# Kernel optimization log

Measured on AMD Instinct MI355X. Metric: run time of the kernel, lower is better.

Reference implementation:

```python
import jax, jax.numpy as jnp
import numpy as np

B, N, FIN, FOUT, OPD = 2048, 64, 96, 128, 48
EPS = 1e-5      # nn.LayerNorm default eps
SLOPE = 0.01    # F.leaky_relu default negative_slope (used in GAT forward)


def setup_inputs() -> dict:
    key = jax.random.key(0)
    ks = jax.random.split(key, 12)
    stdv = 1.0 / np.sqrt(FOUT)
    h = jax.random.normal(ks[0], (B, N, FIN), jnp.float32)
    # binary DAG-style adjacency (float mask, as used multiplicatively in torch)
    adj = (jax.random.uniform(ks[1], (B, N, N)) < 0.3).astype(jnp.float32)
    op_emb = jax.random.normal(ks[2], (B, N, OPD), jnp.float32)
    # DenseGraphFlow params (uniform(-stdv, stdv) per reset_parameters)
    W = jax.random.uniform(ks[3], (FIN, FOUT), jnp.float32, -stdv, stdv)
    b = jax.random.uniform(ks[4], (FOUT,), jnp.float32, -stdv, stdv)
    Wop_d = jax.random.normal(ks[5], (OPD, FOUT), jnp.float32) * 0.05
    bop_d = jnp.zeros((FOUT,), jnp.float32)
    # GraphAttentionLayer params
    Wk = jax.random.normal(ks[6], (FIN, FOUT), jnp.float32) * 0.05
    a_w = jax.random.normal(ks[7], (FOUT,), jnp.float32) * 0.05
    Wop_g = jax.random.normal(ks[8], (OPD, FOUT), jnp.float32) * 0.05
    bop_g = jnp.zeros((FOUT,), jnp.float32)
    gamma = jnp.ones((FOUT,), jnp.float32)
    beta = jnp.zeros((FOUT,), jnp.float32)
    return dict(h=h, adj=adj, op_emb=op_emb, W=W, b=b, Wop_d=Wop_d, bop_d=bop_d,
                Wk=Wk, a_w=a_w, Wop_g=Wop_g, bop_g=bop_g, gamma=gamma, beta=beta)


def reference(h, adj, op_emb, W, b, Wop_d, bop_d, Wk, a_w, Wop_g, bop_g, gamma, beta):
    # ---- DenseGraphFlow (residual=True, opattention=True) ----
    support = jnp.einsum('bnf,fo->bno', h, W)                       # [B,N,FOUT]
    gate_d = jax.nn.sigmoid(op_emb @ Wop_d + bop_d)                 # [B,N,FOUT]
    dense = gate_d * jnp.einsum('bij,bjo->bio', adj, support) + support + b

    # ---- GraphAttentionLayer (unique_attn_proj=False -> Wq=Wv=Wk) ----
    Whk = jnp.einsum('bnf,fo->bno', h, Wk)                          # [B,N,FOUT]
    # torch builds a_input[b,i,j,m] = Whk[b,j,m] * Whk[b,i,m], then projects with
    # a (Linear FOUT->1). Exactly equivalent factored form (no [B,N,N,F] tensor):
    scores = jnp.einsum('bim,bjm->bij', Whk * a_w, Whk)             # [B,N,N]
    alpha = jnp.where(scores >= 0, scores, SLOPE * scores) * adj    # leaky_relu then adj mask
    attn = jax.nn.softmax(alpha, axis=-1)                           # softmax over j (torch dim=-2 of [b,i,j,1])
    hp = jnp.einsum('bij,bjo->bio', attn, Whk)                      # aggregate values
    gate_g = jax.nn.sigmoid(op_emb @ Wop_g + bop_g)
    hp = gate_g * hp
    # LayerNorm over last dim
    mu = jnp.mean(hp, axis=-1, keepdims=True)
    var = jnp.var(hp, axis=-1, keepdims=True)
    hp = (hp - mu) / jnp.sqrt(var + EPS) * gamma + beta

    # ---- ensemble combine ----
    return (dense + hp) / 2
```

## Files before the change

### kernel.cpp

```cpp
#include <hip/hip_runtime.h>

#define NB 2048
#define NN 64
#define KFIN 96
#define KFOUT 128
#define KOPD 48

typedef __attribute__((ext_vector_type(8))) short bf8;
typedef __attribute__((ext_vector_type(4))) float f32x4;
typedef __attribute__((ext_vector_type(4))) unsigned short us4;
typedef __attribute__((ext_vector_type(2))) __bf16 bfx2;

__device__ __forceinline__ unsigned short f2bf(float f) {
  __bf16 h = (__bf16)f;
  return __builtin_bit_cast(unsigned short, h);
}
__device__ __forceinline__ float bf2f(unsigned short s) {
  unsigned int u = ((unsigned int)s) << 16;
  return __builtin_bit_cast(float, u);
}
__device__ __forceinline__ us4 pack4(float a, float b, float c, float d) {
  us4 q; q.x = f2bf(a); q.y = f2bf(b); q.z = f2bf(c); q.w = f2bf(d); return q;
}
__device__ __forceinline__ bf8 pk8(float4 a, float4 b) {
  bf8 r;
  r[0] = (short)f2bf(a.x); r[1] = (short)f2bf(a.y); r[2] = (short)f2bf(a.z); r[3] = (short)f2bf(a.w);
  r[4] = (short)f2bf(b.x); r[5] = (short)f2bf(b.y); r[6] = (short)f2bf(b.z); r[7] = (short)f2bf(b.w);
  return r;
}
__device__ __forceinline__ unsigned int pk2(float lo, float hi) {
  bfx2 v; v[0] = (__bf16)lo; v[1] = (__bf16)hi;
  return __builtin_bit_cast(unsigned int, v);
}
__device__ __forceinline__ float unpk(unsigned int p, int hi) {
  return bf2f((unsigned short)(hi ? (p >> 16) : (p & 0xffffu)));
}

__global__ void prep_weights(const float* __restrict__ W, const float* __restrict__ Wk,
                             const float* __restrict__ Wd, const float* __restrict__ Wg,
                             unsigned short* __restrict__ ws) {
  int idx = blockIdx.x * 256 + threadIdx.x;
  if (idx >= 40960) return;
  float v;
  if (idx < 24576) {
    int r  = (idx < 12288) ? idx : idx - 12288;
    const float* M = (idx < 12288) ? W : Wk;
    int nb = r / 1536, rem = r % 1536;
    int kb = rem / 512, rem2 = rem % 512;
    int l = rem2 >> 3, e = rem2 & 7;
    int o = nb * 16 + (l & 15);
    int k = kb * 32 + (l >> 4) * 8 + e;
    v = M[k * 128 + o];
  } else {
    int r  = (idx < 32768) ? idx - 24576 : idx - 32768;
    const float* M = (idx < 32768) ? Wd : Wg;
    int nb = r / 1024, rem = r % 1024;
    int kb = rem / 512, rem2 = rem % 512;
    int l = rem2 >> 3, e = rem2 & 7;
    int o = nb * 16 + (l & 15);
    int k = kb * 32 + (l >> 4) * 8 + e;
    v = (k < 48) ? M[k * 128 + o] : 0.f;
  }
  ws[idx] = f2bf(v);
}

#define LD1 68
#define LD2 132
#define LDA 68
__global__ __launch_bounds__(256, 4) void gin_fused(
    const float* __restrict__ hg, const float* __restrict__ adjg,
    const float* __restrict__ opeg, const float* __restrict__ bvec,
    const float* __restrict__ bopd, const float* __restrict__ bopg,
    const float* __restrict__ awv, const float* __restrict__ gmv,
    const float* __restrict__ btv, const unsigned short* __restrict__ ws,
    float* __restrict__ out) {
  __shared__ __align__(16) char smem[34304];
  unsigned short* buf1 = (unsigned short*)smem;
  unsigned short* buf2 = (unsigned short*)(smem + 17408);

  const int t  = threadIdx.x;
  const int b  = blockIdx.x;
  const int w  = t >> 6;
  const int l  = t & 63;
  const int lr = l & 15;
  const int lg = l >> 4;
  const int kcol = 8 * lg;
  const int arow = w * 16 + lr;
  const int rowb = w * 16 + lg * 4;

  const float* hrow = hg   + (size_t)b * (NN * KFIN) + arow * KFIN;
  const float* orow = opeg + (size_t)b * (NN * KOPD) + arow * KOPD;
  float* outp = out + (size_t)b * (NN * KFOUT);

  const unsigned short* WT  = ws;
  const unsigned short* WkT = ws + 12288;
  const unsigned short* WdT = ws + 24576;
  const unsigned short* WgT = ws + 32768;
  f32x4 zz = {0.f, 0.f, 0.f, 0.f};

  bf8 oa[2], ha[3];
  {
    float4 p0 = *(const float4*)(orow + kcol);
    float4 p1 = *(const float4*)(orow + kcol + 4);
    oa[0] = pk8(p0, p1);
    if (lg < 2) {
      float4 q0 = *(const float4*)(orow + 32 + kcol);
      float4 q1 = *(const float4*)(orow + 32 + kcol + 4);
      oa[1] = pk8(q0, q1);
    } else {
      bf8 z = {0, 0, 0, 0, 0, 0, 0, 0};
      oa[1] = z;
    }
  }
  #pragma unroll
  for (int kb = 0; kb < 3; ++kb) {
    float4 p0 = *(const float4*)(hrow + kb * 32 + kcol);
    float4 p1 = *(const float4*)(hrow + kb * 32 + kcol + 4);
    ha[kb] = pk8(p0, p1);
  }

  unsigned int gdp[8][2];
  {
    f32x4 gd[8] = {zz, zz, zz, zz, zz, zz, zz, zz};
    #pragma unroll
    for (int kb = 0; kb < 2; ++kb) {
      #pragma unroll
      for (int nb = 0; nb < 8; ++nb) {
        bf8 bb = *(const bf8*)(WdT + (nb * 2 + kb) * 512 + l * 8);
        gd[nb] = __builtin_amdgcn_mfma_f32_16x16x32_bf16(oa[kb], bb, gd[nb], 0, 0, 0);
      }
    }
    #pragma unroll
    for (int nb = 0; nb < 8; ++nb) {
      float bo = bopd[nb * 16 + lr];
      float g0 = 1.f / (1.f + __expf(-(gd[nb][0] + bo)));
      float g1 = 1.f / (1.f + __expf(-(gd[nb][1] + bo)));
      float g2 = 1.f / (1.f + __expf(-(gd[nb][2] + bo)));
      float g3 = 1.f / (1.f + __expf(-(gd[nb][3] + bo)));
      gdp[nb][0] = pk2(g0, g1); gdp[nb][1] = pk2(g2, g3);
    }
  }

  f32x4 sacc[8] = {zz, zz, zz, zz, zz, zz, zz, zz};
  #pragma unroll
  for (int kb = 0; kb < 3; ++kb) {
    #pragma unroll
    for (int nb = 0; nb < 8; ++nb) {
      bf8 bb = *(const bf8*)(WT + (nb * 3 + kb) * 512 + l * 8);
      sacc[nb] = __builtin_amdgcn_mfma_f32_16x16x32_bf16(ha[kb], bb, sacc[nb], 0, 0, 0);
    }
  }
  #pragma unroll
  for (int nb = 0; nb < 8; ++nb)
    *(us4*)(buf1 + (nb * 16 + lr) * LD1 + w * 16 + lg * 4) =
        pack4(sacc[nb][0], sacc[nb][1], sacc[nb][2], sacc[nb][3]);
  __syncthreads();

  unsigned int dnp[8][2];
  {
    const float* ajr = adjg + (size_t)b * (NN * NN) + arow * NN;
    bf8 aa[2];
    #pragma unroll
    for (int kb = 0; kb < 2; ++kb) {
      float4 p0 = *(const float4*)(ajr + kb * 32 + kcol);
      float4 p1 = *(const float4*)(ajr + kb * 32 + kcol + 4);
      aa[kb] = pk8(p0, p1);
    }
    #pragma unroll
    for (int nb = 0; nb < 8; ++nb) {
      f32x4 dacc = zz;
      #pragma unroll
      for (int kb = 0; kb < 2; ++kb) {
        bf8 bb = *(const bf8*)(buf1 + (nb * 16 + lr) * LD1 + kb * 32 + kcol);
        dacc = __builtin_amdgcn_mfma_f32_16x16x32_bf16(aa[kb], bb, dacc, 0, 0, 0);
      }
      float bc = bvec[nb * 16 + lr];
      float d0 = unpk(gdp[nb][0], 0) * dacc[0] + sacc[nb][0] + bc;
      float d1 = unpk(gdp[nb][0], 1) * dacc[1] + sacc[nb][1] + bc;
      float d2 = unpk(gdp[nb][1], 0) * dacc[2] + sacc[nb][2] + bc;
      float d3 = unpk(gdp[nb][1], 1) * dacc[3] + sacc[nb][3] + bc;
      dnp[nb][0] = pk2(d0, d1); dnp[nb][1] = pk2(d2, d3);
    }
  }

  f32x4 wacc[8] = {zz, zz, zz, zz, zz, zz, zz, zz};
  #pragma unroll
  for (int kb = 0; kb < 3; ++kb) {
    #pragma unroll
    for (int nb = 0; nb < 8; ++nb) {
      bf8 bb = *(const bf8*)(WkT + (nb * 3 + kb) * 512 + l * 8);
      wacc[nb] = __builtin_amdgcn_mfma_f32_16x16x32_bf16(ha[kb], bb, wacc[nb], 0, 0, 0);
    }
  }
  __syncthreads();

  #pragma unroll
  for (int nb = 0; nb < 8; ++nb) {
    int o = nb * 16 + lr;
    *(us4*)(buf1 + o * LD1 + w * 16 + lg * 4) =
        pack4(wacc[nb][0], wacc[nb][1], wacc[nb][2], wacc[nb][3]);
    #pragma unroll
    for (int r = 0; r < 4; ++r)
      buf2[(w * 16 + lg * 4 + r) * LD2 + o] = f2bf(wacc[nb][r]);
  }

  unsigned int ggp[8][2];
  {
    f32x4 gg[8] = {zz, zz, zz, zz, zz, zz, zz, zz};
    #pragma unroll
    for (int kb = 0; kb < 2; ++kb) {
      #pragma unroll
      for (int nb = 0; nb < 8; ++nb) {
        bf8 bb = *(const bf8*)(WgT + (nb * 2 + kb) * 512 + l * 8);
        gg[nb] = __builtin_amdgcn_mfma_f32_16x16x32_bf16(oa[kb], bb, gg[nb], 0, 0, 0);
      }
    }
    #pragma unroll
    for (int nb = 0; nb < 8; ++nb) {
      float bo = bopg[nb * 16 + lr];
      float g0 = 1.f / (1.f + __expf(-(gg[nb][0] + bo)));
      float g1 = 1.f / (1.f + __expf(-(gg[nb][1] + bo)));
      float g2 = 1.f / (1.f + __expf(-(gg[nb][2] + bo)));
      float g3 = 1.f / (1.f + __expf(-(gg[nb][3] + bo)));
      ggp[nb][0] = pk2(g0, g1); ggp[nb][1] = pk2(g2, g3);
    }
  }
  __syncthreads();

  f32x4 sc[4] = {zz, zz, zz, zz};
  #pragma unroll
  for (int kb = 0; kb < 4; ++kb) {
    bf8 ar = *(const bf8*)(buf2 + arow * LD2 + kb * 32 + kcol);
    const float4* ap = (const float4*)(awv + kb * 32 + kcol);
    float4 a0 = ap[0], a1 = ap[1];
    bf8 a;
    a[0] = (short)f2bf(bf2f((unsigned short)ar[0]) * a0.x);
    a[1] = (short)f2bf(bf2f((unsigned short)ar[1]) * a0.y);
    a[2] = (short)f2bf(bf2f((unsigned short)ar[2]) * a0.z);
    a[3] = (short)f2bf(bf2f((unsigned short)ar[3]) * a0.w);
    a[4] = (short)f2bf(bf2f((unsigned short)ar[4]) * a1.x);
    a[5] = (short)f2bf(bf2f((unsigned short)ar[5]) * a1.y);
    a[6] = (short)f2bf(bf2f((unsigned short)ar[6]) * a1.z);
    a[7] = (short)f2bf(bf2f((unsigned short)ar[7]) * a1.w);
    #pragma unroll
    for (int jb = 0; jb < 4; ++jb) {
      bf8 bb = *(const bf8*)(buf2 + (jb * 16 + lr) * LD2 + kb * 32 + kcol);
      sc[jb] = __builtin_amdgcn_mfma_f32_16x16x32_bf16(a, bb, sc[jb], 0, 0, 0);
    }
  }

  float al[4][4];
  #pragma unroll
  for (int jb = 0; jb < 4; ++jb)
    #pragma unroll
    for (int r = 0; r < 4; ++r) {
      float am = adjg[(size_t)b * (NN * NN) + (rowb + r) * NN + jb * 16 + lr];
      float s = sc[jb][r];
      al[jb][r] = (s >= 0.f ? s : 0.01f * s) * am;
    }
  #pragma unroll
  for (int r = 0; r < 4; ++r) {
    float m = fmaxf(fmaxf(al[0][r], al[1][r]), fmaxf(al[2][r], al[3][r]));
    m = fmaxf(m, __shfl_xor(m, 1));
    m = fmaxf(m, __shfl_xor(m, 2));
    m = fmaxf(m, __shfl_xor(m, 4));
    m = fmaxf(m, __shfl_xor(m, 8));
    float s0 = 0.f;
    #pragma unroll
    for (int jb = 0; jb < 4; ++jb) { float p = __expf(al[jb][r] - m); al[jb][r] = p; s0 += p; }
    s0 += __shfl_xor(s0, 1);
    s0 += __shfl_xor(s0, 2);
    s0 += __shfl_xor(s0, 4);
    s0 += __shfl_xor(s0, 8);
    float inv = 1.f / s0;
    #pragma unroll
    for (int jb = 0; jb < 4; ++jb) al[jb][r] *= inv;
  }
  __syncthreads();

  unsigned short* attn_s = buf2;
  #pragma unroll
  for (int jb = 0; jb < 4; ++jb)
    #pragma unroll
    for (int r = 0; r < 4; ++r)
      attn_s[(rowb + r) * LDA + jb * 16 + lr] = f2bf(al[jb][r]);

  f32x4 hpacc[8] = {zz, zz, zz, zz, zz, zz, zz, zz};
  #pragma unroll
  for (int kb = 0; kb < 2; ++kb) {
    bf8 a = *(const bf8*)(attn_s + arow * LDA + kb * 32 + kcol);
    #pragma unroll
    for (int nb = 0; nb < 8; ++nb) {
      bf8 bb = *(const bf8*)(buf1 + (nb * 16 + lr) * LD1 + kb * 32 + kcol);
      hpacc[nb] = __builtin_amdgcn_mfma_f32_16x16x32_bf16(a, bb, hpacc[nb], 0, 0, 0);
    }
  }

  float gam[8], bet[8];
  #pragma unroll
  for (int nb = 0; nb < 8; ++nb) { gam[nb] = gmv[nb * 16 + lr]; bet[nb] = btv[nb * 16 + lr]; }
  #pragma unroll
  for (int r = 0; r < 4; ++r) {
    float hv[8]; float su = 0.f, sq = 0.f;
    #pragma unroll
    for (int nb = 0; nb < 8; ++nb) {
      float v = unpk(ggp[nb][r >> 1], r & 1) * hpacc[nb][r];
      hv[nb] = v; su += v; sq += v * v;
    }
    su += __shfl_xor(su, 1); su += __shfl_xor(su, 2);
    su += __shfl_xor(su, 4); su += __shfl_xor(su, 8);
    sq += __shfl_xor(sq, 1); sq += __shfl_xor(sq, 2);
    sq += __shfl_xor(sq, 4); sq += __shfl_xor(sq, 8);
    float mean = su * (1.f / 128.f);
    float var  = sq * (1.f / 128.f) - mean * mean;
    float rinv = rsqrtf(var + 1e-5f);
    int row = rowb + r;
    #pragma unroll
    for (int nb = 0; nb < 8; ++nb) {
      float hn = (hv[nb] - mean) * rinv * gam[nb] + bet[nb];
      float dv = unpk(dnp[nb][r >> 1], r & 1);
      outp[row * 128 + nb * 16 + lr] = (dv + hn) * 0.5f;
    }
  }
}

extern "C" void kernel_launch(void* const* d_in, const int* in_sizes, int n_in,
                              void* d_out, int out_size, void* d_ws, size_t ws_size,
                              hipStream_t stream) {
  const float* h     = (const float*)d_in[0];
  const float* adj   = (const float*)d_in[1];
  const float* ope   = (const float*)d_in[2];
  const float* W     = (const float*)d_in[3];
  const float* bvec  = (const float*)d_in[4];
  const float* Wopd  = (const float*)d_in[5];
  const float* bopd  = (const float*)d_in[6];
  const float* Wk    = (const float*)d_in[7];
  const float* a_w   = (const float*)d_in[8];
  const float* Wopg  = (const float*)d_in[9];
  const float* bopg  = (const float*)d_in[10];
  const float* gamma = (const float*)d_in[11];
  const float* beta  = (const float*)d_in[12];
  float* out = (float*)d_out;
  unsigned short* ws = (unsigned short*)d_ws;

  prep_weights<<<dim3(160), dim3(256), 0, stream>>>(W, Wk, Wopd, Wopg, ws);
  gin_fused<<<dim3(NB), dim3(256), 0, stream>>>(h, adj, ope, bvec, bopd, bopg,
                                                a_w, gamma, beta, ws, out);
}
```

Measured before the change: 103.2 us.

## Shrink shared memory by dropping transposed Whk copy to raise occupancy

Keeps only the row-major bf16 copy of Whk in shared memory and builds the B operand of the attention-times-values MFMA with strided scalar LDS reads. Attention weights get their own small region, which cuts shared memory from about 34 KB to 26 KB and removes one barrier. Launch bounds rise to 5 blocks per CU. The adjacency mask loads are hoisted before the score MFMAs, and the sigmoid and softmax divides use the fast rcp builtin. The trade is more LDS instructions, with possible bank conflicts, in the hp MFMA loop and tighter register limits in exchange for more resident waves.

```diff
diff --git a/kernel.cpp b/kernel.cpp
--- a/kernel.cpp
+++ b/kernel.cpp
@@ -34,6 +34,9 @@
 }
 __device__ __forceinline__ float unpk(unsigned int p, int hi) {
   return bf2f((unsigned short)(hi ? (p >> 16) : (p & 0xffffu)));
+}
+__device__ __forceinline__ float sigm(float x) {
+  return __builtin_amdgcn_rcpf(1.f + __expf(-x));
 }
 
 __global__ void prep_weights(const float* __restrict__ W, const float* __restrict__ Wk,
@@ -67,16 +70,16 @@
 #define LD1 68
 #define LD2 132
 #define LDA 68
-__global__ __launch_bounds__(256, 4) void gin_fused(
+__global__ __launch_bounds__(256, 5) void gin_fused(
     const float* __restrict__ hg, const float* __restrict__ adjg,
     const float* __restrict__ opeg, const float* __restrict__ bvec,
     const float* __restrict__ bopd, const float* __restrict__ bopg,
     const float* __restrict__ awv, const float* __restrict__ gmv,
     const float* __restrict__ btv, const unsigned short* __restrict__ ws,
     float* __restrict__ out) {
-  __shared__ __align__(16) char smem[34304];
-  unsigned short* buf1 = (unsigned short*)smem;
-  unsigned short* buf2 = (unsigned short*)(smem + 17408);
+  __shared__ __align__(16) char smem[26112];
+  unsigned short* buf1   = (unsigned short*)smem;
+  unsigned short* attn_s = (unsigned short*)(smem + 17408);
 
   const int t  = threadIdx.x;
   const int b  = blockIdx.x;
@@ -133,11 +136,8 @@
     #pragma unroll
     for (int nb = 0; nb < 8; ++nb) {
       float bo = bopd[nb * 16 + lr];
-      float g0 = 1.f / (1.f + __expf(-(gd[nb][0] + bo)));
-      float g1 = 1.f / (1.f + __expf(-(gd[nb][1] + bo)));
-      float g2 = 1.f / (1.f + __expf(-(gd[nb][2] + bo)));
-      float g3 = 1.f / (1.f + __expf(-(gd[nb][3] + bo)));
-      gdp[nb][0] = pk2(g0, g1); gdp[nb][1] = pk2(g2, g3);
+      gdp[nb][0] = pk2(sigm(gd[nb][0] + bo), sigm(gd[nb][1] + bo));
+      gdp[nb][1] = pk2(sigm(gd[nb][2] + bo), sigm(gd[nb][3] + bo));
     }
   }
 
@@ -197,11 +197,9 @@
   #pragma unroll
   for (int nb = 0; nb < 8; ++nb) {
     int o = nb * 16 + lr;
-    *(us4*)(buf1 + o * LD1 + w * 16 + lg * 4) =
-        pack4(wacc[nb][0], wacc[nb][1], wacc[nb][2], wacc[nb][3]);
     #pragma unroll
     for (int r = 0; r < 4; ++r)
-      buf2[(w * 16 + lg * 4 + r) * LD2 + o] = f2bf(wacc[nb][r]);
+      buf1[(w * 16 + lg * 4 + r) * LD2 + o] = f2bf(wacc[nb][r]);
   }
 
   unsigned int ggp[8][2];
@@ -218,19 +216,24 @@
     #pragma unroll
     for (int nb = 0; nb < 8; ++nb) {
       float bo = bopg[nb * 16 + lr];
-      float g0 = 1.f / (1.f + __expf(-(gg[nb][0] + bo)));
-      float g1 = 1.f / (1.f + __expf(-(gg[nb][1] + bo)));
-      float g2 = 1.f / (1.f + __expf(-(gg[nb][2] + bo)));
-      float g3 = 1.f / (1.f + __expf(-(gg[nb][3] + bo)));
-      ggp[nb][0] = pk2(g0, g1); ggp[nb][1] = pk2(g2, g3);
-    }
-  }
+      ggp[nb][0] = pk2(sigm(gg[nb][0] + bo), sigm(gg[nb][1] + bo));
+      ggp[nb][1] = pk2(sigm(gg[nb][2] + bo), sigm(gg[nb][3] + bo));
+    }
+  }
+
+  float msk[4][4];
+  #pragma unroll
+  for (int jb = 0; jb < 4; ++jb)
+    #pragma unroll
+    for (int r = 0; r < 4; ++r)
+      msk[jb][r] = adjg[(size_t)b * (NN * NN) + (rowb + r) * NN + jb * 16 + lr];
+
   __syncthreads();
 
   f32x4 sc[4] = {zz, zz, zz, zz};
   #pragma unroll
   for (int kb = 0; kb < 4; ++kb) {
-    bf8 ar = *(const bf8*)(buf2 + arow * LD2 + kb * 32 + kcol);
+    bf8 ar = *(const bf8*)(buf1 + arow * LD2 + kb * 32 + kcol);
     const float4* ap = (const float4*)(awv + kb * 32 + kcol);
     float4 a0 = ap[0], a1 = ap[1];
     bf8 a;
@@ -244,7 +247,7 @@
     a[7] = (short)f2bf(bf2f((unsigned short)ar[7]) * a1.w);
     #pragma unroll
     for (int jb = 0; jb < 4; ++jb) {
-      bf8 bb = *(const bf8*)(buf2 + (jb * 16 + lr) * LD2 + kb * 32 + kcol);
+      bf8 bb = *(const bf8*)(buf1 + (jb * 16 + lr) * LD2 + kb * 32 + kcol);
       sc[jb] = __builtin_amdgcn_mfma_f32_16x16x32_bf16(a, bb, sc[jb], 0, 0, 0);
     }
   }
@@ -254,9 +257,8 @@
   for (int jb = 0; jb < 4; ++jb)
     #pragma unroll
     for (int r = 0; r < 4; ++r) {
-      float am = adjg[(size_t)b * (NN * NN) + (rowb + r) * NN + jb * 16 + lr];
       float s = sc[jb][r];
-      al[jb][r] = (s >= 0.f ? s : 0.01f * s) * am;
+      al[jb][r] = (s >= 0.f ? s : 0.01f * s) * msk[jb][r];
     }
   #pragma unroll
   for (int r = 0; r < 4; ++r) {
@@ -272,13 +274,11 @@
     s0 += __shfl_xor(s0, 2);
     s0 += __shfl_xor(s0, 4);
     s0 += __shfl_xor(s0, 8);
-    float inv = 1.f / s0;
+    float inv = __builtin_amdgcn_rcpf(s0);
     #pragma unroll
     for (int jb = 0; jb < 4; ++jb) al[jb][r] *= inv;
   }
-  __syncthreads();
-
-  unsigned short* attn_s = buf2;
+
   #pragma unroll
   for (int jb = 0; jb < 4; ++jb)
     #pragma unroll
@@ -291,7 +291,10 @@
     bf8 a = *(const bf8*)(attn_s + arow * LDA + kb * 32 + kcol);
     #pragma unroll
     for (int nb = 0; nb < 8; ++nb) {
-      bf8 bb = *(const bf8*)(buf1 + (nb * 16 + lr) * LD1 + kb * 32 + kcol);
+      const unsigned short* gp = buf1 + (kb * 32 + 8 * lg) * LD2 + nb * 16 + lr;
+      bf8 bb;
+      #pragma unroll
+      for (int e = 0; e < 8; ++e) bb[e] = (short)gp[e * LD2];
       hpacc[nb] = __builtin_amdgcn_mfma_f32_16x16x32_bf16(a, bb, hpacc[nb], 0, 0, 0);
     }
   }
```

After: 121.4 us. 17.6% more time.
